# Kernel tuning notes

Hardware: AMD Instinct MI355X
Metric: run time of the kernel (lower is better)

The kernel has to match this reference:

```python
import jax, jax.numpy as jnp
import numpy as np
import math

B, S, D, H = 2, 2048, 768, 12
HD = D // H


def setup_inputs() -> dict:
    key = jax.random.key(0)
    ks = jax.random.split(key, 9)
    scale = 1.0 / math.sqrt(D)
    x = jax.random.normal(ks[0], (B, S, D), dtype=jnp.float32)
    # causal mask: True where attention is allowed (query i attends to key j<=i)
    mask = jnp.tril(jnp.ones((S, S), dtype=bool))[None, None]  # [1,1,S,S]
    wq = jax.random.normal(ks[1], (D, D), dtype=jnp.float32) * scale
    bq = jnp.zeros((D,), dtype=jnp.float32)
    wk = jax.random.normal(ks[2], (D, D), dtype=jnp.float32) * scale
    bk = jnp.zeros((D,), dtype=jnp.float32)
    wv = jax.random.normal(ks[3], (D, D), dtype=jnp.float32) * scale
    bv = jnp.zeros((D,), dtype=jnp.float32)
    wo = jax.random.normal(ks[4], (D, D), dtype=jnp.float32) * scale
    bo = jnp.zeros((D,), dtype=jnp.float32)
    return {"x": x, "mask": mask, "wq": wq, "bq": bq, "wk": wk, "bk": bk,
            "wv": wv, "bv": bv, "wo": wo, "bo": bo}


def reference(x, mask, wq, bq, wk, bk, wv, bv, wo, bo):
    b, s, d = x.shape
    # projections (flax Linear: y = x @ kernel + bias)
    q = (x @ wq + bq).reshape(b, s, H, HD).transpose(0, 2, 1, 3)  # [b,h,s,hd]
    k = (x @ wk + bk).reshape(b, s, H, HD).transpose(0, 2, 1, 3)
    v = (x @ wv + bv).reshape(b, s, H, HD).transpose(0, 2, 1, 3)
    scores = jnp.einsum('bhqd,bhkd->bhqk', q, k) / math.sqrt(HD)  # [b,h,s,s]
    scores = jnp.where(mask, scores, -jnp.inf)
    attn = jax.nn.softmax(scores, axis=-1)
    out = jnp.einsum('bhqk,bhkd->bhqd', attn, v)  # [b,h,s,hd]
    out = out.transpose(0, 2, 1, 3).reshape(b, s, d)
    return out @ wo + bo
```

## Files before the change

kernel.cpp:

```cpp
#include <hip/hip_runtime.h>
#include <math.h>

#define BATCH 2
#define SEQ   2048
#define DMODEL 768
#define NHEAD 12
#define HDIM  64

typedef unsigned short u16;
typedef __attribute__((ext_vector_type(8))) short bf16x8;
typedef __attribute__((ext_vector_type(4))) float f32x4;
typedef __attribute__((ext_vector_type(16))) float f32x16;
typedef __attribute__((ext_vector_type(8))) unsigned short us8;
typedef __attribute__((ext_vector_type(4))) unsigned short us4;

__device__ __forceinline__ u16 f2bf(float f) {
    union { float f; unsigned u; } v; v.f = f;
    unsigned u = v.u;
    u += 0x7fff + ((u >> 16) & 1);
    return (u16)(u >> 16);
}

__device__ __forceinline__ float fexp2(float x) {
#if __has_builtin(__builtin_amdgcn_exp2f)
    return __builtin_amdgcn_exp2f(x);
#else
    return exp2f(x);
#endif
}

__device__ __forceinline__ void g2l16(const void* g, void* l) {
    __builtin_amdgcn_global_load_lds(
        (const __attribute__((address_space(1))) unsigned int*)g,
        (__attribute__((address_space(3))) unsigned int*)(unsigned int)(unsigned long long)(uintptr_t)l,
        16, 0, 0);
}

__device__ __forceinline__ void stage_rows(const u16* g, u16* lds, int nrows,
                                           int tid) {
    const int row = tid >> 2, col = (tid & 3) * 8;
    g2l16(g + (size_t)row * DMODEL + col, lds + tid * 8);
    if (nrows == 128) {
        g2l16(g + (size_t)(row + 64) * DMODEL + col, lds + 2048 + tid * 8);
    } else if (nrows == 96) {
        if (tid < 128)
            g2l16(g + (size_t)(row + 64) * DMODEL + col, lds + 2048 + tid * 8);
    }
}

__global__ __launch_bounds__(256) void prep(const float* __restrict__ x,
                                            const float* __restrict__ w0,
                                            const float* __restrict__ w1,
                                            const float* __restrict__ w2,
                                            const float* __restrict__ w3,
                                            u16* __restrict__ xb,
                                            u16* __restrict__ Wt_all) {
    __shared__ float t[32][33];
    const int bid = blockIdx.x;
    if (bid < 3072) {
        int i = bid * 256 + threadIdx.x;
        float4 v = ((const float4*)x)[i];
        us4 o;
        o.x = f2bf(v.x); o.y = f2bf(v.y); o.z = f2bf(v.z); o.w = f2bf(v.w);
        *(us4*)&xb[(size_t)i * 4] = o;
    } else {
        const int wid = bid - 3072;
        const int z  = wid / 576;
        const int rr = wid % 576;
        const int by = rr / 24, bx = rr % 24;
        const float* W = z == 0 ? w0 : z == 1 ? w1 : z == 2 ? w2 : w3;
        u16* Wt = Wt_all + (size_t)z * DMODEL * DMODEL;

        int tx = threadIdx.x & 31, ty = threadIdx.x >> 5;
        int xg = bx * 32 + tx;
        #pragma unroll
        for (int j = 0; j < 32; j += 8)
            t[ty + j][tx] = W[(size_t)(by * 32 + ty + j) * DMODEL + xg];
        __syncthreads();
        int x2 = by * 32 + tx;
        #pragma unroll
        for (int j = 0; j < 32; j += 8)
            Wt[(size_t)(bx * 32 + ty + j) * DMODEL + x2] = f2bf(t[tx][ty + j]);
    }
}

__global__ __launch_bounds__(256) void gemm_qkv(
    const u16* __restrict__ xb, const u16* __restrict__ WtQK,
    const u16* __restrict__ WtV,
    const float* __restrict__ bq, const float* __restrict__ bk,
    const float* __restrict__ bv,
    u16* __restrict__ QK, u16* __restrict__ Vt) {

    __shared__ __align__(16) u16 As[128 * 32];
    __shared__ __align__(16) u16 Bs[128 * 32];

    const int tid  = threadIdx.x;
    const int lane = tid & 63;
    const int w    = tid >> 6;
    const int quad = lane >> 4, l16 = lane & 15;
    const int wm   = w >> 1, wn = w & 1;
    const int b    = blockIdx.x;

    if (b < 512) {
        const int m0 = (b >> 4) * 128;
        const int n0 = (b & 15) * 96;
        f32x4 acc[4][3] = {};
        for (int k0 = 0; k0 < DMODEL; k0 += 32) {
            stage_rows(xb   + (size_t)m0 * DMODEL + k0, As, 128, tid);
            stage_rows(WtQK + (size_t)n0 * DMODEL + k0, Bs,  96, tid);
            __syncthreads();
            bf16x8 af[4], bfr[3];
            #pragma unroll
            for (int i = 0; i < 4; ++i)
                af[i] = *(const bf16x8*)&As[(wm * 64 + i * 16 + l16) * 32 + quad * 8];
            #pragma unroll
            for (int j = 0; j < 3; ++j)
                bfr[j] = *(const bf16x8*)&Bs[(wn * 48 + j * 16 + l16) * 32 + quad * 8];
            #pragma unroll
            for (int i = 0; i < 4; ++i)
                #pragma unroll
                for (int j = 0; j < 3; ++j)
                    acc[i][j] = __builtin_amdgcn_mfma_f32_16x16x32_bf16(af[i], bfr[j], acc[i][j], 0, 0, 0);
            __syncthreads();
        }
        const size_t n_elem = (size_t)BATCH * SEQ * DMODEL;
        #pragma unroll
        for (int j = 0; j < 3; ++j) {
            const int n     = n0 + wn * 48 + j * 16 + l16;
            const int which = n / 768;
            const int nn    = n - which * 768;
            const float bias  = (which == 0 ? bq : bk)[nn];
            const float scale = (which == 0) ? 0.18033688011112043f : 1.0f;
            const int h = nn >> 6, hd = nn & 63;
            u16* outw = QK + (size_t)which * n_elem;
            #pragma unroll
            for (int i = 0; i < 4; ++i) {
                const int mbase = m0 + wm * 64 + i * 16 + quad * 4;
                #pragma unroll
                for (int r = 0; r < 4; ++r) {
                    const int m  = mbase + r;
                    const int b_ = m >> 11, s_ = m & 2047;
                    outw[(size_t)((b_ * NHEAD + h) * SEQ + s_) * HDIM + hd] =
                        f2bf((acc[i][j][r] + bias) * scale);
                }
            }
        }
    } else {
        const int vj = b - 512;
        const int m0 = (vj & 7) * 96;
        const int n0 = (vj >> 3) * 128;
        f32x4 acc[3][4] = {};
        for (int k0 = 0; k0 < DMODEL; k0 += 32) {
            stage_rows(WtV + (size_t)m0 * DMODEL + k0, As,  96, tid);
            stage_rows(xb  + (size_t)n0 * DMODEL + k0, Bs, 128, tid);
            __syncthreads();
            bf16x8 af[3], bfr[4];
            #pragma unroll
            for (int i = 0; i < 3; ++i)
                af[i] = *(const bf16x8*)&As[(wm * 48 + i * 16 + l16) * 32 + quad * 8];
            #pragma unroll
            for (int j = 0; j < 4; ++j)
                bfr[j] = *(const bf16x8*)&Bs[(wn * 64 + j * 16 + l16) * 32 + quad * 8];
            #pragma unroll
            for (int i = 0; i < 3; ++i)
                #pragma unroll
                for (int j = 0; j < 4; ++j)
                    acc[i][j] = __builtin_amdgcn_mfma_f32_16x16x32_bf16(af[i], bfr[j], acc[i][j], 0, 0, 0);
            __syncthreads();
        }
        #pragma unroll
        for (int i = 0; i < 3; ++i) {
            const int rbase = m0 + wm * 48 + i * 16 + quad * 4;
            #pragma unroll
            for (int r = 0; r < 4; ++r) {
                const int row_g = rbase + r;
                const float bias = bv[row_g];
                const int h = row_g >> 6, hd = row_g & 63;
                #pragma unroll
                for (int j = 0; j < 4; ++j) {
                    const int col_g = n0 + wn * 64 + j * 16 + l16;
                    const int b_ = col_g >> 11, s_ = col_g & 2047;
                    Vt[(size_t)((b_ * NHEAD + h) * HDIM + hd) * SEQ + s_] =
                        f2bf(acc[i][j][r] + bias);
                }
            }
        }
    }
}

__global__ __launch_bounds__(256) void gemm_out(
    const u16* __restrict__ Ag, const u16* __restrict__ Bt,
    const float* __restrict__ bo, float* __restrict__ out) {

    __shared__ __align__(16) u16 As[64 * 32];
    __shared__ __align__(16) u16 Bs[64 * 32];

    const int tid  = threadIdx.x;
    const int lane = tid & 63;
    const int w    = tid >> 6;
    const int quad = lane >> 4, l16 = lane & 15;
    const int wm   = w >> 1, wn = w & 1;
    const int m0 = blockIdx.x * 64, n0 = blockIdx.y * 64;

    const int rowA = tid >> 2;
    const int kch  = (tid & 3) * 8;

    f32x4 acc[2][2] = {};

    for (int k0 = 0; k0 < DMODEL; k0 += 32) {
        g2l16(Ag + (size_t)(m0 + rowA) * DMODEL + k0 + kch, As + tid * 8);
        g2l16(Bt + (size_t)(n0 + rowA) * DMODEL + k0 + kch, Bs + tid * 8);
        __syncthreads();

        bf16x8 af[2], bfr[2];
        #pragma unroll
        for (int i = 0; i < 2; ++i)
            af[i] = *(const bf16x8*)&As[(wm * 32 + i * 16 + l16) * 32 + quad * 8];
        #pragma unroll
        for (int j = 0; j < 2; ++j)
            bfr[j] = *(const bf16x8*)&Bs[(wn * 32 + j * 16 + l16) * 32 + quad * 8];
        #pragma unroll
        for (int i = 0; i < 2; ++i)
            #pragma unroll
            for (int j = 0; j < 2; ++j)
                acc[i][j] = __builtin_amdgcn_mfma_f32_16x16x32_bf16(af[i], bfr[j], acc[i][j], 0, 0, 0);
        __syncthreads();
    }

    #pragma unroll
    for (int i = 0; i < 2; ++i) {
        const int mbase = m0 + wm * 32 + i * 16 + quad * 4;
        #pragma unroll
        for (int r = 0; r < 4; ++r) {
            const int m = mbase + r;
            #pragma unroll
            for (int j = 0; j < 2; ++j) {
                const int n = n0 + wn * 32 + j * 16 + l16;
                out[(size_t)m * DMODEL + n] = acc[i][j][r] + bo[n];
            }
        }
    }
}

__global__ __launch_bounds__(128) void flash_attn_mfma(
    const u16* __restrict__ Q, const u16* __restrict__ K,
    const u16* __restrict__ Vt, u16* __restrict__ A) {

    __shared__ __align__(16) u16 Kl[3][64 * 64];
    __shared__ __align__(16) u16 Vl[3][64 * 64];

    const int tid  = threadIdx.x;
    const int lane = tid & 63;
    const int w    = tid >> 6;
    const int l32  = lane & 31;
    const int hi   = lane >> 5;

    const int sid = 767 - (int)blockIdx.x;
    const int j   = sid / 24;
    const int bh  = sid - j * 24;
    const int tc  = j + 1;

    const size_t base = (size_t)bh * SEQ * HDIM;
    const u16* Qg = Q + base;
    const u16* Kg = K + base;
    const u16* Vg = Vt + base;

    const int wq0   = j * 64 + w * 32;
    const int wlast = wq0 + 31;
    const int qg    = wq0 + l32;

    bf16x8 qf[4];
    #pragma unroll
    for (int c = 0; c < 4; ++c)
        qf[c] = *(const bf16x8*)&Qg[(size_t)qg * 64 + 16 * c + 8 * hi];

    f32x16 o0 = {}, o1 = {};
    float l_acc = 0.f;

    const u16* kp[4]; const u16* vp[4];
    #pragma unroll
    for (int i = 0; i < 4; ++i) {
        const int ch = tid + i * 128;
        const int r  = ch >> 3, lc = (ch & 7) ^ (r & 7);
        kp[i] = Kg + (size_t)r * 64 + lc * 8;
        vp[i] = Vg + (size_t)r * SEQ + lc * 8;
    }

    auto STAGE = [&](int buf) {
        #pragma unroll
        for (int i = 0; i < 4; ++i) {
            const int ch = tid + i * 128;
            g2l16(kp[i], &Kl[buf][ch * 8]);
            g2l16(vp[i], &Vl[buf][ch * 8]);
            kp[i] += 64 * 64;
            vp[i] += 64;
        }
    };

    STAGE(0);
    if (tc > 1) STAGE(1);

    int cur = 0, nb = 2;
    const int cx = l32 & 7;
    for (int t = 0; t < tc; ++t) {
        if (t + 1 < tc) asm volatile("s_waitcnt vmcnt(8)" ::: "memory");
        else            asm volatile("s_waitcnt vmcnt(0)" ::: "memory");
        __builtin_amdgcn_s_barrier();
        if (t + 2 < tc) { STAGE(nb); nb = (nb == 2) ? 0 : nb + 1; }

        const u16* Kc = Kl[cur];
        const u16* Vc = Vl[cur];
        const int j0 = t * 64;
        const bool do1 = (j0 + 32 <= wlast);

        f32x16 s0 = {}, s1 = {};
        __builtin_amdgcn_s_setprio(1);
        #pragma unroll
        for (int c = 0; c < 4; ++c) {
            bf16x8 kf = *(const bf16x8*)&Kc[l32 * 64 + (((2 * c + hi) ^ cx) * 8)];
            s0 = __builtin_amdgcn_mfma_f32_32x32x16_bf16(kf, qf[c], s0, 0, 0, 0);
        }
        if (do1) {
            #pragma unroll
            for (int c = 0; c < 4; ++c) {
                bf16x8 kf = *(const bf16x8*)&Kc[(32 + l32) * 64 + (((2 * c + hi) ^ cx) * 8)];
                s1 = __builtin_amdgcn_mfma_f32_32x32x16_bf16(kf, qf[c], s1, 0, 0, 0);
            }
        }
        __builtin_amdgcn_s_setprio(0);

        if (t == tc - 1) {
            #pragma unroll
            for (int r = 0; r < 16; ++r) {
                const int key = j0 + (r & 3) + 8 * (r >> 2) + 4 * hi;
                if (key > qg) s0[r] = -INFINITY;
            }
            if (do1) {
                #pragma unroll
                for (int r = 0; r < 16; ++r) {
                    const int key = j0 + 32 + (r & 3) + 8 * (r >> 2) + 4 * hi;
                    if (key > qg) s1[r] = -INFINITY;
                }
            }
        }

        #pragma unroll
        for (int r = 0; r < 16; ++r) s0[r] = fexp2(s0[r]);
        if (do1) {
            #pragma unroll
            for (int r = 0; r < 16; ++r) s1[r] = fexp2(s1[r]);
        }
        float ps = 0.f;
        #pragma unroll
        for (int r = 0; r < 16; ++r) ps += s0[r] + s1[r];
        l_acc += ps;

        bf16x8 pa[4];
        #pragma unroll
        for (int kw = 0; kw < 4; ++kw) {
            const f32x16& sv = (kw < 2) ? s0 : s1;
            const int m0i = 2 * (kw & 1);
            unsigned a0l, a0h, a1l, a1h;
            asm("v_cvt_pk_bf16_f32 %0, %1, %2" : "=v"(a0l) : "v"(sv[4 * m0i + 0]), "v"(sv[4 * m0i + 1]));
            asm("v_cvt_pk_bf16_f32 %0, %1, %2" : "=v"(a0h) : "v"(sv[4 * m0i + 2]), "v"(sv[4 * m0i + 3]));
            asm("v_cvt_pk_bf16_f32 %0, %1, %2" : "=v"(a1l) : "v"(sv[4 * (m0i + 1) + 0]), "v"(sv[4 * (m0i + 1) + 1]));
            asm("v_cvt_pk_bf16_f32 %0, %1, %2" : "=v"(a1h) : "v"(sv[4 * (m0i + 1) + 2]), "v"(sv[4 * (m0i + 1) + 3]));
            asm("v_permlane32_swap_b32 %0, %1" : "+v"(a0l), "+v"(a1l));
            asm("v_permlane32_swap_b32 %0, %1" : "+v"(a0h), "+v"(a1h));
            union { unsigned u[4]; bf16x8 v; } pu;
            pu.u[0] = a0l; pu.u[1] = a0h; pu.u[2] = a1l; pu.u[3] = a1h;
            pa[kw] = pu.v;
        }

        __builtin_amdgcn_s_setprio(1);
        #pragma unroll
        for (int kw = 0; kw < 4; ++kw) {
            const int pc = ((2 * kw + hi) ^ cx) * 8;
            bf16x8 vf0 = *(const bf16x8*)&Vc[l32 * 64 + pc];
            bf16x8 vf1 = *(const bf16x8*)&Vc[(32 + l32) * 64 + pc];
            o0 = __builtin_amdgcn_mfma_f32_32x32x16_bf16(vf0, pa[kw], o0, 0, 0, 0);
            o1 = __builtin_amdgcn_mfma_f32_32x32x16_bf16(vf1, pa[kw], o1, 0, 0, 0);
        }
        __builtin_amdgcn_s_setprio(0);

        cur = (cur == 2) ? 0 : cur + 1;
    }

    __syncthreads();

    const float tot = l_acc + __shfl_xor(l_acc, 32);
    const float inv = 1.0f / tot;

    u16* Ot = ((u16*)Kl) + w * 2304;
    #pragma unroll
    for (int r = 0; r < 16; ++r) {
        const int d = (r & 3) + 8 * (r >> 2) + 4 * hi;
        Ot[l32 * 72 + d]      = f2bf(o0[r] * inv);
        Ot[l32 * 72 + 32 + d] = f2bf(o1[r] * inv);
    }
    const int row = lane >> 1, d0 = (lane & 1) * 32;
    const int b_ = bh / NHEAD, h_ = bh % NHEAD;
    u16* dst = A + ((size_t)(b_ * SEQ + wq0 + row)) * DMODEL + h_ * HDIM + d0;
    #pragma unroll
    for (int k2 = 0; k2 < 4; ++k2)
        *(us8*)&dst[k2 * 8] = *(const us8*)&Ot[row * 72 + d0 + k2 * 8];
}

extern "C" void kernel_launch(void* const* d_in, const int* in_sizes, int n_in,
                              void* d_out, int out_size, void* d_ws, size_t ws_size,
                              hipStream_t stream) {
    const float* x  = (const float*)d_in[0];
    const float* wq = (const float*)d_in[2];
    const float* bq = (const float*)d_in[3];
    const float* wk = (const float*)d_in[4];
    const float* bk = (const float*)d_in[5];
    const float* wv = (const float*)d_in[6];
    const float* bv = (const float*)d_in[7];
    const float* wo = (const float*)d_in[8];
    const float* bo = (const float*)d_in[9];
    float* out = (float*)d_out;

    const size_t n_elem = (size_t)BATCH * SEQ * DMODEL;
    const size_t w_elem = (size_t)DMODEL * DMODEL;

    u16* xb     = (u16*)d_ws;
    u16* Wt_all = xb + n_elem;
    u16* Qw     = Wt_all + 4 * w_elem;
    u16* Vtw    = Qw + 2 * n_elem;
    u16* Aw     = Vtw + n_elem;

    dim3 blk(256);

    prep<<<dim3(3072 + 2304), blk, 0, stream>>>(x, wq, wk, wv, wo, xb, Wt_all);

    gemm_qkv<<<dim3(768), blk, 0, stream>>>(xb, Wt_all, Wt_all + 2 * w_elem,
                                            bq, bk, bv, Qw, Vtw);

    flash_attn_mfma<<<dim3(768), dim3(128), 0, stream>>>(Qw, Qw + n_elem, Vtw, Aw);

    gemm_out<<<dim3(64, 12), blk, 0, stream>>>(Aw, Wt_all + 3 * w_elem, bo, out);
}
```

Measured before the change: 171.7 us.

## Split flash-attention key tiles across four waves with cross-wave output reduction

Doubles the attention block from two to four waves: each pair of waves now handles half of every 64-key tile (kh) for one 32-query half (qh), instead of one wave processing the full key tile. Partial outputs and row sums from the kh=1 waves are reduced through shared memory before normalization and store. This is meant to raise per-CU wave parallelism and shorten each wave's serial dependency chain, and the load work per thread is halved. The cost is an extra LDS reduction with a barrier at the end, and the already-masked upper-half key tile on the diagonal is skipped by one wave, which leaves it idle.

```diff
diff --git a/kernel.cpp b/kernel.cpp
--- a/kernel.cpp
+++ b/kernel.cpp
@@ -242,7 +242,7 @@
     }
 }
 
-__global__ __launch_bounds__(128) void flash_attn_mfma(
+__global__ __launch_bounds__(256) void flash_attn_mfma(
     const u16* __restrict__ Q, const u16* __restrict__ K,
     const u16* __restrict__ Vt, u16* __restrict__ A) {
 
@@ -254,6 +254,8 @@
     const int w    = tid >> 6;
     const int l32  = lane & 31;
     const int hi   = lane >> 5;
+    const int qh   = w & 1;
+    const int kh   = w >> 1;
 
     const int sid = 767 - (int)blockIdx.x;
     const int j   = sid / 24;
@@ -265,9 +267,8 @@
     const u16* Kg = K + base;
     const u16* Vg = Vt + base;
 
-    const int wq0   = j * 64 + w * 32;
-    const int wlast = wq0 + 31;
-    const int qg    = wq0 + l32;
+    const int wq0 = j * 64 + qh * 32;
+    const int qg  = wq0 + l32;
 
     bf16x8 qf[4];
     #pragma unroll
@@ -277,24 +278,21 @@
     f32x16 o0 = {}, o1 = {};
     float l_acc = 0.f;
 
-    const u16* kp[4]; const u16* vp[4];
-    #pragma unroll
-    for (int i = 0; i < 4; ++i) {
-        const int ch = tid + i * 128;
-        const int r  = ch >> 3, lc = (ch & 7) ^ (r & 7);
-        kp[i] = Kg + (size_t)r * 64 + lc * 8;
-        vp[i] = Vg + (size_t)r * SEQ + lc * 8;
-    }
+    const int ch0 = tid, ch1 = tid + 256;
+    const int r0 = ch0 >> 3, lc0 = (ch0 & 7) ^ (r0 & 7);
+    const int r1 = ch1 >> 3, lc1 = (ch1 & 7) ^ (r1 & 7);
+    const u16* kp0 = Kg + (size_t)r0 * 64 + lc0 * 8;
+    const u16* kp1 = Kg + (size_t)r1 * 64 + lc1 * 8;
+    const u16* vp0 = Vg + (size_t)r0 * SEQ + lc0 * 8;
+    const u16* vp1 = Vg + (size_t)r1 * SEQ + lc1 * 8;
 
     auto STAGE = [&](int buf) {
-        #pragma unroll
-        for (int i = 0; i < 4; ++i) {
-            const int ch = tid + i * 128;
-            g2l16(kp[i], &Kl[buf][ch * 8]);
-            g2l16(vp[i], &Vl[buf][ch * 8]);
-            kp[i] += 64 * 64;
-            vp[i] += 64;
-        }
+        g2l16(kp0, &Kl[buf][ch0 * 8]);
+        g2l16(kp1, &Kl[buf][ch1 * 8]);
+        g2l16(vp0, &Vl[buf][ch0 * 8]);
+        g2l16(vp1, &Vl[buf][ch1 * 8]);
+        kp0 += 64 * 64; kp1 += 64 * 64;
+        vp0 += 64;      vp1 += 64;
     };
 
     STAGE(0);
@@ -303,107 +301,110 @@
     int cur = 0, nb = 2;
     const int cx = l32 & 7;
     for (int t = 0; t < tc; ++t) {
-        if (t + 1 < tc) asm volatile("s_waitcnt vmcnt(8)" ::: "memory");
+        if (t + 1 < tc) asm volatile("s_waitcnt vmcnt(4)" ::: "memory");
         else            asm volatile("s_waitcnt vmcnt(0)" ::: "memory");
         __builtin_amdgcn_s_barrier();
         if (t + 2 < tc) { STAGE(nb); nb = (nb == 2) ? 0 : nb + 1; }
 
-        const u16* Kc = Kl[cur];
-        const u16* Vc = Vl[cur];
-        const int j0 = t * 64;
-        const bool do1 = (j0 + 32 <= wlast);
-
-        f32x16 s0 = {}, s1 = {};
-        __builtin_amdgcn_s_setprio(1);
-        #pragma unroll
-        for (int c = 0; c < 4; ++c) {
-            bf16x8 kf = *(const bf16x8*)&Kc[l32 * 64 + (((2 * c + hi) ^ cx) * 8)];
-            s0 = __builtin_amdgcn_mfma_f32_32x32x16_bf16(kf, qf[c], s0, 0, 0, 0);
-        }
-        if (do1) {
+        const bool live = !(t == tc - 1 && qh == 0 && kh == 1);
+        if (live) {
+            const u16* Kc = Kl[cur];
+            const u16* Vc = Vl[cur];
+            const int j0 = t * 64;
+
+            f32x16 s = {};
+            __builtin_amdgcn_s_setprio(1);
             #pragma unroll
             for (int c = 0; c < 4; ++c) {
-                bf16x8 kf = *(const bf16x8*)&Kc[(32 + l32) * 64 + (((2 * c + hi) ^ cx) * 8)];
-                s1 = __builtin_amdgcn_mfma_f32_32x32x16_bf16(kf, qf[c], s1, 0, 0, 0);
-            }
-        }
-        __builtin_amdgcn_s_setprio(0);
-
-        if (t == tc - 1) {
-            #pragma unroll
-            for (int r = 0; r < 16; ++r) {
-                const int key = j0 + (r & 3) + 8 * (r >> 2) + 4 * hi;
-                if (key > qg) s0[r] = -INFINITY;
-            }
-            if (do1) {
+                bf16x8 kf = *(const bf16x8*)&Kc[(32 * kh + l32) * 64 + (((2 * c + hi) ^ cx) * 8)];
+                s = __builtin_amdgcn_mfma_f32_32x32x16_bf16(kf, qf[c], s, 0, 0, 0);
+            }
+            __builtin_amdgcn_s_setprio(0);
+
+            if (t == tc - 1) {
                 #pragma unroll
                 for (int r = 0; r < 16; ++r) {
-                    const int key = j0 + 32 + (r & 3) + 8 * (r >> 2) + 4 * hi;
-                    if (key > qg) s1[r] = -INFINITY;
+                    const int key = j0 + 32 * kh + (r & 3) + 8 * (r >> 2) + 4 * hi;
+                    if (key > qg) s[r] = -INFINITY;
                 }
             }
-        }
-
-        #pragma unroll
-        for (int r = 0; r < 16; ++r) s0[r] = fexp2(s0[r]);
-        if (do1) {
-            #pragma unroll
-            for (int r = 0; r < 16; ++r) s1[r] = fexp2(s1[r]);
-        }
-        float ps = 0.f;
-        #pragma unroll
-        for (int r = 0; r < 16; ++r) ps += s0[r] + s1[r];
-        l_acc += ps;
-
-        bf16x8 pa[4];
-        #pragma unroll
-        for (int kw = 0; kw < 4; ++kw) {
-            const f32x16& sv = (kw < 2) ? s0 : s1;
-            const int m0i = 2 * (kw & 1);
-            unsigned a0l, a0h, a1l, a1h;
-            asm("v_cvt_pk_bf16_f32 %0, %1, %2" : "=v"(a0l) : "v"(sv[4 * m0i + 0]), "v"(sv[4 * m0i + 1]));
-            asm("v_cvt_pk_bf16_f32 %0, %1, %2" : "=v"(a0h) : "v"(sv[4 * m0i + 2]), "v"(sv[4 * m0i + 3]));
-            asm("v_cvt_pk_bf16_f32 %0, %1, %2" : "=v"(a1l) : "v"(sv[4 * (m0i + 1) + 0]), "v"(sv[4 * (m0i + 1) + 1]));
-            asm("v_cvt_pk_bf16_f32 %0, %1, %2" : "=v"(a1h) : "v"(sv[4 * (m0i + 1) + 2]), "v"(sv[4 * (m0i + 1) + 3]));
-            asm("v_permlane32_swap_b32 %0, %1" : "+v"(a0l), "+v"(a1l));
-            asm("v_permlane32_swap_b32 %0, %1" : "+v"(a0h), "+v"(a1h));
-            union { unsigned u[4]; bf16x8 v; } pu;
-            pu.u[0] = a0l; pu.u[1] = a0h; pu.u[2] = a1l; pu.u[3] = a1h;
-            pa[kw] = pu.v;
-        }
-
-        __builtin_amdgcn_s_setprio(1);
-        #pragma unroll
-        for (int kw = 0; kw < 4; ++kw) {
-            const int pc = ((2 * kw + hi) ^ cx) * 8;
-            bf16x8 vf0 = *(const bf16x8*)&Vc[l32 * 64 + pc];
-            bf16x8 vf1 = *(const bf16x8*)&Vc[(32 + l32) * 64 + pc];
-            o0 = __builtin_amdgcn_mfma_f32_32x32x16_bf16(vf0, pa[kw], o0, 0, 0, 0);
-            o1 = __builtin_amdgcn_mfma_f32_32x32x16_bf16(vf1, pa[kw], o1, 0, 0, 0);
-        }
-        __builtin_amdgcn_s_setprio(0);
+
+            #pragma unroll
+            for (int r = 0; r < 16; ++r) s[r] = fexp2(s[r]);
+            float ps = 0.f;
+            #pragma unroll
+            for (int r = 0; r < 16; ++r) ps += s[r];
+            l_acc += ps;
+
+            bf16x8 pa[2];
+            #pragma unroll
+            for (int kw = 0; kw < 2; ++kw) {
+                const int m0i = 2 * kw;
+                unsigned a0l, a0h, a1l, a1h;
+                asm("v_cvt_pk_bf16_f32 %0, %1, %2" : "=v"(a0l) : "v"(s[4 * m0i + 0]), "v"(s[4 * m0i + 1]));
+                asm("v_cvt_pk_bf16_f32 %0, %1, %2" : "=v"(a0h) : "v"(s[4 * m0i + 2]), "v"(s[4 * m0i + 3]));
+                asm("v_cvt_pk_bf16_f32 %0, %1, %2" : "=v"(a1l) : "v"(s[4 * (m0i + 1) + 0]), "v"(s[4 * (m0i + 1) + 1]));
+                asm("v_cvt_pk_bf16_f32 %0, %1, %2" : "=v"(a1h) : "v"(s[4 * (m0i + 1) + 2]), "v"(s[4 * (m0i + 1) + 3]));
+                asm("v_permlane32_swap_b32 %0, %1" : "+v"(a0l), "+v"(a1l));
+                asm("v_permlane32_swap_b32 %0, %1" : "+v"(a0h), "+v"(a1h));
+                union { unsigned u[4]; bf16x8 v; } pu;
+                pu.u[0] = a0l; pu.u[1] = a0h; pu.u[2] = a1l; pu.u[3] = a1h;
+                pa[kw] = pu.v;
+            }
+
+            __builtin_amdgcn_s_setprio(1);
+            #pragma unroll
+            for (int kw = 0; kw < 2; ++kw) {
+                const int lc = ((4 * kh + 2 * kw + hi) ^ cx) * 8;
+                bf16x8 vf0 = *(const bf16x8*)&Vc[l32 * 64 + lc];
+                bf16x8 vf1 = *(const bf16x8*)&Vc[(32 + l32) * 64 + lc];
+                o0 = __builtin_amdgcn_mfma_f32_32x32x16_bf16(vf0, pa[kw], o0, 0, 0, 0);
+                o1 = __builtin_amdgcn_mfma_f32_32x32x16_bf16(vf1, pa[kw], o1, 0, 0, 0);
+            }
+            __builtin_amdgcn_s_setprio(0);
+        }
 
         cur = (cur == 2) ? 0 : cur + 1;
     }
 
+    l_acc += __shfl_xor(l_acc, 32);
+
     __syncthreads();
 
-    const float tot = l_acc + __shfl_xor(l_acc, 32);
-    const float inv = 1.0f / tot;
-
-    u16* Ot = ((u16*)Kl) + w * 2304;
-    #pragma unroll
-    for (int r = 0; r < 16; ++r) {
-        const int d = (r & 3) + 8 * (r >> 2) + 4 * hi;
-        Ot[l32 * 72 + d]      = f2bf(o0[r] * inv);
-        Ot[l32 * 72 + 32 + d] = f2bf(o1[r] * inv);
-    }
-    const int row = lane >> 1, d0 = (lane & 1) * 32;
-    const int b_ = bh / NHEAD, h_ = bh % NHEAD;
-    u16* dst = A + ((size_t)(b_ * SEQ + wq0 + row)) * DMODEL + h_ * HDIM + d0;
-    #pragma unroll
-    for (int k2 = 0; k2 < 4; ++k2)
-        *(us8*)&dst[k2 * 8] = *(const us8*)&Ot[row * 72 + d0 + k2 * 8];
+    float* ob = (float*)Kl;
+    float* lb = (float*)Vl;
+    if (kh == 1) {
+        #pragma unroll
+        for (int r = 0; r < 16; ++r) {
+            ob[qh * 2048 + r * 64 + lane]        = o0[r];
+            ob[qh * 2048 + (16 + r) * 64 + lane] = o1[r];
+        }
+        lb[qh * 64 + lane] = l_acc;
+    }
+    __syncthreads();
+
+    if (kh == 0) {
+        #pragma unroll
+        for (int r = 0; r < 16; ++r) {
+            o0[r] += ob[qh * 2048 + r * 64 + lane];
+            o1[r] += ob[qh * 2048 + (16 + r) * 64 + lane];
+        }
+        const float inv = 1.0f / (l_acc + lb[qh * 64 + lane]);
+
+        u16* Ot = ((u16*)Vl) + 256 + qh * 2304;
+        #pragma unroll
+        for (int r = 0; r < 16; ++r) {
+            const int d = (r & 3) + 8 * (r >> 2) + 4 * hi;
+            Ot[l32 * 72 + d]      = f2bf(o0[r] * inv);
+            Ot[l32 * 72 + 32 + d] = f2bf(o1[r] * inv);
+        }
+        const int row = lane >> 1, d0 = (lane & 1) * 32;
+        const int b_ = bh / NHEAD, h_ = bh % NHEAD;
+        u16* dst = A + ((size_t)(b_ * SEQ + wq0 + row)) * DMODEL + h_ * HDIM + d0;
+        #pragma unroll
+        for (int k2 = 0; k2 < 4; ++k2)
+            *(us8*)&dst[k2 * 8] = *(const us8*)&Ot[row * 72 + d0 + k2 * 8];
+    }
 }
 
 extern "C" void kernel_launch(void* const* d_in, const int* in_sizes, int n_in,
@@ -436,7 +437,7 @@
     gemm_qkv<<<dim3(768), blk, 0, stream>>>(xb, Wt_all, Wt_all + 2 * w_elem,
                                             bq, bk, bv, Qw, Vtw);
 
-    flash_attn_mfma<<<dim3(768), dim3(128), 0, stream>>>(Qw, Qw + n_elem, Vtw, Aw);
+    flash_attn_mfma<<<dim3(768), blk, 0, stream>>>(Qw, Qw + n_elem, Vtw, Aw);
 
     gemm_out<<<dim3(64, 12), blk, 0, stream>>>(Aw, Wt_all + 3 * w_elem, bo, out);
 }
```

Measured after the change: 159.9 us. 1.07x faster.
